# Optimization experiments

Measured on AMD Instinct MI355X. Metric: run time of the kernel, lower is better.

The kernel has to match this reference:

```python
import jax, jax.numpy as jnp
import numpy as np
import math

B, S, E, H, FF = 2, 2048, 1024, 16, 4096
HD = E // H
EPS = 1e-6


def layer_norm(x, gamma, beta):
    mu = jnp.mean(x, axis=-1, keepdims=True)
    var = jnp.mean(jnp.square(x - mu), axis=-1, keepdims=True)
    return (x - mu) * jax.lax.rsqrt(var + EPS) * gamma + beta


def setup_inputs() -> dict:
    key = jax.random.key(0)
    ks = jax.random.split(key, 8)
    x_embeds = jax.random.normal(ks[0], (B, S, E), dtype=jnp.float32)
    # causal mask: True means masked (j > i), broadcastable over batch/heads
    mask = jnp.triu(jnp.ones((S, S), dtype=bool), k=1)[None, None]
    sc = 1.0 / math.sqrt(E)
    w_kqv = jax.random.normal(ks[1], (3 * E, E), dtype=jnp.float32) * sc
    w_o = jax.random.normal(ks[2], (E, E), dtype=jnp.float32) * sc
    w_up = jax.random.normal(ks[3], (FF, E), dtype=jnp.float32) * sc
    b_up = jnp.zeros((FF,), dtype=jnp.float32)
    w_down = jax.random.normal(ks[4], (E, FF), dtype=jnp.float32) / math.sqrt(FF)
    b_down = jnp.zeros((E,), dtype=jnp.float32)
    g1 = jnp.ones((E,), dtype=jnp.float32)
    b1 = jnp.zeros((E,), dtype=jnp.float32)
    g2 = jnp.ones((E,), dtype=jnp.float32)
    b2 = jnp.zeros((E,), dtype=jnp.float32)
    return {"x_embeds": x_embeds, "mask": mask, "w_kqv": w_kqv, "w_o": w_o,
            "w_up": w_up, "b_up": b_up, "w_down": w_down, "b_down": b_down,
            "g1": g1, "b1": b1, "g2": g2, "b2": b2}


def reference(x_embeds, mask, w_kqv, w_o, w_up, b_up, w_down, b_down, g1, b1, g2, b2):
    b, s = x_embeds.shape[0], x_embeds.shape[1]
    # --- attention ---
    kqv = x_embeds @ w_kqv.T                      # [B,S,3E]
    kqv = kqv.reshape(b, s, 3, H, HD).transpose(0, 3, 2, 1, 4)  # [B,H,3,S,HD]
    xk, xq, xv = kqv[:, :, 0], kqv[:, :, 1], kqv[:, :, 2]
    attn = jnp.einsum('bhqd,bhkd->bhqk', xq, xk) / math.sqrt(HD)
    attn = jnp.where(mask, -jnp.inf, attn)
    attn = jax.nn.softmax(attn, axis=-1)
    out = jnp.einsum('bhqk,bhkd->bhqd', attn, xv)  # [B,H,S,HD]
    out = out.transpose(0, 2, 1, 3).reshape(b, s, E)
    out = out @ w_o.T
    x = layer_norm(out + x_embeds, g1, b1)
    # --- ffnn ---
    h = jax.nn.relu(x @ w_up.T + b_up)
    h = h @ w_down.T + b_down
    return layer_norm(h + x, g2, b2)
```

## Files before the change

### kernel.cpp

```cpp
#include <hip/hip_runtime.h>
#include <stdint.h>

#define B_ 2
#define S_ 2048
#define E_ 1024
#define H_ 16
#define HD_ 64
#define FF_ 4096
#define M_ 4096
#define LOG2E_ 1.44269504f

typedef short bf16x8 __attribute__((ext_vector_type(8)));
typedef float f32x4  __attribute__((ext_vector_type(4)));
typedef short shortx4 __attribute__((ext_vector_type(4)));

#define MFMA16(a,b,c) __builtin_amdgcn_mfma_f32_16x16x32_bf16(a,b,c,0,0,0)

__device__ __forceinline__ short f2bf(float f) {
  uint32_t u = __builtin_bit_cast(uint32_t, f);
  u += 0x7fffu + ((u >> 16) & 1u);
  return (short)(u >> 16);
}
__device__ __forceinline__ float bf2f(short b) {
  uint32_t u = ((uint32_t)(uint16_t)b) << 16;
  return __builtin_bit_cast(float, u);
}
__device__ __forceinline__ float exp2_hw(float x) {
  float r;
  asm("v_exp_f32 %0, %1" : "=v"(r) : "v"(x));
  return r;
}

template<int CTRL>
__device__ __forceinline__ float dpp_ror(float x) {
  return __builtin_bit_cast(float,
    __builtin_amdgcn_update_dpp(0, __builtin_bit_cast(int, x), CTRL, 0xF, 0xF, true));
}
__device__ __forceinline__ float dpp_max16(float v) {
  v = fmaxf(v, dpp_ror<0x128>(v));
  v = fmaxf(v, dpp_ror<0x124>(v));
  v = fmaxf(v, dpp_ror<0x122>(v));
  v = fmaxf(v, dpp_ror<0x121>(v));
  return v;
}
__device__ __forceinline__ float dpp_sum16(float v) {
  v += dpp_ror<0x128>(v);
  v += dpp_ror<0x124>(v);
  v += dpp_ror<0x122>(v);
  v += dpp_ror<0x121>(v);
  return v;
}

#define GLDS16(g, l) __builtin_amdgcn_global_load_lds( \
    (const __attribute__((address_space(1))) unsigned int*)(g), \
    (__attribute__((address_space(3))) unsigned int*)(l), 16, 0, 0)

__global__ void cast_all(const float* __restrict__ x, const float* __restrict__ wkqv,
                         const float* __restrict__ wo, const float* __restrict__ wup,
                         const float* __restrict__ wdown,
                         short* __restrict__ xb, short* __restrict__ wkqvb,
                         short* __restrict__ wob, short* __restrict__ wupb,
                         short* __restrict__ wdownb) {
  const int stride = gridDim.x * blockDim.x;
  for (int i = blockIdx.x * blockDim.x + threadIdx.x; i < 4194304; i += stride) {
    const int e = i << 2;
    const float* src; short* dst; int off;
    if (e < 4194304)       { src = x;     dst = xb;     off = e; }
    else if (e < 7340032)  { src = wkqv;  dst = wkqvb;  off = e - 4194304; }
    else if (e < 8388608)  { src = wo;    dst = wob;    off = e - 7340032; }
    else if (e < 12582912) { src = wup;   dst = wupb;   off = e - 8388608; }
    else                   { src = wdown; dst = wdownb; off = e - 12582912; }
    float4 v = *(const float4*)(src + off);
    shortx4 o;
    o.x = f2bf(v.x); o.y = f2bf(v.y); o.z = f2bf(v.z); o.w = f2bf(v.w);
    *(shortx4*)(dst + off) = o;
  }
}

template<int SK, int EPI, typename OutT>
__global__ __launch_bounds__(256) void gemm_bt(
    const short* __restrict__ A, const short* __restrict__ Bw,
    OutT* __restrict__ C0, OutT* __restrict__ C1, const float* __restrict__ bias,
    int M, int N, int K)
{
  __shared__ short Al[2][128 * 32];
  __shared__ short Bl[2][128 * 32];
  const int tid  = threadIdx.x;
  const int w    = tid >> 6, lane = tid & 63;
  const int ntiles = N >> 7;
  const int nwg = gridDim.x;
  const int bid = blockIdx.x;
  const int swz = (bid & 7) * (nwg >> 3) + (bid >> 3);
  const int tn = swz % ntiles, tm = swz / ntiles;
  const int m0 = tm << 7, n0 = tn << 7;
  const int wr = (w >> 1) << 6, wc = (w & 1) << 6;
  const int lr = lane & 15, lk = (lane >> 4) << 3;
  const int ra = lane >> 2, colA = (lane & 3) << 3;

  const int kper = K / SK;
  const int kbeg = (SK > 1) ? (int)blockIdx.y * kper : 0;
  const int T = kper >> 5;
  OutT* __restrict__ C = (SK > 1 && blockIdx.y) ? C1 : C0;

  const short* Ag0 = A  + (size_t)(m0 + w * 16 + ra) * K + colA;
  const short* Ag1 = A  + (size_t)(m0 + (w + 4) * 16 + ra) * K + colA;
  const short* Bg0 = Bw + (size_t)(n0 + w * 16 + ra) * K + colA;
  const short* Bg1 = Bw + (size_t)(n0 + (w + 4) * 16 + ra) * K + colA;

  f32x4 acc[4][4] = {};

  {
    const int k0 = kbeg;
    GLDS16(Ag0 + k0, &Al[0][w * 512]);
    GLDS16(Ag1 + k0, &Al[0][(w + 4) * 512]);
    GLDS16(Bg0 + k0, &Bl[0][w * 512]);
    GLDS16(Bg1 + k0, &Bl[0][(w + 4) * 512]);
  }

  for (int it = 0; it < T; ++it) {
    const int buf = it & 1;
    if (it + 1 < T) {
      const int k1 = kbeg + ((it + 1) << 5);
      GLDS16(Ag0 + k1, &Al[buf ^ 1][w * 512]);
      GLDS16(Ag1 + k1, &Al[buf ^ 1][(w + 4) * 512]);
      GLDS16(Bg0 + k1, &Bl[buf ^ 1][w * 512]);
      GLDS16(Bg1 + k1, &Bl[buf ^ 1][(w + 4) * 512]);
      asm volatile("s_waitcnt vmcnt(4)" ::: "memory");
    } else {
      asm volatile("s_waitcnt vmcnt(0)" ::: "memory");
    }
    __builtin_amdgcn_sched_barrier(0);
    __builtin_amdgcn_s_barrier();

    bf16x8 af[4], bfr[4];
    #pragma unroll
    for (int i = 0; i < 4; ++i)
      af[i] = *(const bf16x8*)&Al[buf][(wr + i * 16 + lr) * 32 + lk];
    #pragma unroll
    for (int j = 0; j < 4; ++j)
      bfr[j] = *(const bf16x8*)&Bl[buf][(wc + j * 16 + lr) * 32 + lk];
    #pragma unroll
    for (int i = 0; i < 4; ++i)
      #pragma unroll
      for (int j = 0; j < 4; ++j)
        acc[i][j] = MFMA16(af[i], bfr[j], acc[i][j]);

    __builtin_amdgcn_s_barrier();
  }

  const int lg = lane >> 4;
  #pragma unroll
  for (int j = 0; j < 4; ++j) {
    const int col = n0 + wc + j * 16 + lr;
    float bv = 0.f;
    if constexpr (SK == 1 && EPI != 0) bv = bias[col];
    #pragma unroll
    for (int i = 0; i < 4; ++i) {
      #pragma unroll
      for (int r = 0; r < 4; ++r) {
        const int row = m0 + wr + i * 16 + lg * 4 + r;
        float v = acc[i][j][r] + bv;
        if constexpr (SK == 1 && EPI == 1) v = fmaxf(v, 0.f);
        if constexpr (sizeof(OutT) == 2) C[(size_t)row * N + col] = f2bf(v);
        else                             C[(size_t)row * N + col] = v;
      }
    }
  }
}

__global__ __launch_bounds__(256) void attn_kernel(
    const short* __restrict__ kqv, short* __restrict__ out)
{
  __shared__ short Kt[64][72];
  __shared__ short Vt[64][72];
  __shared__ short Pl[4][16][72];

  const int tid = threadIdx.x, w = tid >> 6, lane = tid & 63;
  const int p = blockIdx.x;
  const int bh = blockIdx.y;
  const int b = bh >> 4, h = bh & 15;
  const int q0lo = p << 6, q0hi = (31 - p) << 6;
  const int nkb = 32 - p;
  const int lr = lane & 15, lg = lane >> 4;

  const size_t rowlo = (size_t)(b * S_ + q0lo + w * 16 + lr) * 3072 + 1024 + h * 64;
  const size_t rowhi = (size_t)(b * S_ + q0hi + w * 16 + lr) * 3072 + 1024 + h * 64;
  bf16x8 qlo[2], qhi[2];
  qlo[0] = *(const bf16x8*)&kqv[rowlo + lg * 8];
  qlo[1] = *(const bf16x8*)&kqv[rowlo + 32 + lg * 8];
  qhi[0] = *(const bf16x8*)&kqv[rowhi + lg * 8];
  qhi[1] = *(const bf16x8*)&kqv[rowhi + 32 + lg * 8];
  #pragma unroll
  for (int ks = 0; ks < 2; ++ks)
    #pragma unroll
    for (int e = 0; e < 8; ++e) {
      qlo[ks][e] = f2bf(bf2f(qlo[ks][e]) * 0.125f);
      qhi[ks][e] = f2bf(bf2f(qhi[ks][e]) * 0.125f);
    }

  f32x4 aclo[4] = {}, achi[4] = {};
  float mlo[4], llo[4], mhi[4], lhi[4];
  #pragma unroll
  for (int r = 0; r < 4; ++r) { mlo[r] = mhi[r] = -1e30f; llo[r] = lhi[r] = 0.f; }

  const int skk = tid >> 3;
  const int sc  = (tid & 7) << 3;
  const int vws = (tid & 7) << 3;

  for (int kbi = 0; kbi < nkb; ++kbi) {
    const int kb = kbi << 6;
    #pragma unroll
    for (int i = 0; i < 2; ++i) {
      const int krow = skk + i * 32;
      const size_t gb = (size_t)(b * S_ + kb + krow) * 3072 + h * 64 + sc;
      *(bf16x8*)&Kt[krow][sc] = *(const bf16x8*)&kqv[gb];
      bf16x8 vv = *(const bf16x8*)&kqv[gb + 2048];
      const int kc = krow ^ vws;
      #pragma unroll
      for (int e = 0; e < 8; ++e) Vt[sc + e][kc] = vv[e];
    }
    __syncthreads();

    auto process = [&](const bf16x8 (&qf)[2], f32x4 (&acc)[4],
                       float (&m_run)[4], float (&l_run)[4], int q0) {
      f32x4 sacc[4] = {};
      __builtin_amdgcn_s_setprio(1);
      #pragma unroll
      for (int jt = 0; jt < 4; ++jt) {
        #pragma unroll
        for (int ks = 0; ks < 2; ++ks) {
          bf16x8 kf = *(const bf16x8*)&Kt[jt * 16 + lr][ks * 32 + lg * 8];
          sacc[jt] = MFMA16(qf[ks], kf, sacc[jt]);
        }
      }
      __builtin_amdgcn_s_setprio(0);
      const bool full = (kb + 63 <= q0 + w * 16);
      float rmax[4];
      if (full) {
        #pragma unroll
        for (int r = 0; r < 4; ++r)
          rmax[r] = fmaxf(fmaxf(sacc[0][r], sacc[1][r]), fmaxf(sacc[2][r], sacc[3][r]));
      } else {
        #pragma unroll
        for (int r = 0; r < 4; ++r) rmax[r] = -1e30f;
        #pragma unroll
        for (int jt = 0; jt < 4; ++jt) {
          const int kpos = kb + jt * 16 + lr;
          #pragma unroll
          for (int r = 0; r < 4; ++r) {
            const int qrow = q0 + w * 16 + lg * 4 + r;
            float v = (kpos <= qrow) ? sacc[jt][r] : -1e30f;
            sacc[jt][r] = v;
            rmax[r] = fmaxf(rmax[r], v);
          }
        }
      }
      #pragma unroll
      for (int r = 0; r < 4; ++r) rmax[r] = dpp_max16(rmax[r]);
      int need = 0;
      #pragma unroll
      for (int r = 0; r < 4; ++r) need |= (rmax[r] > m_run[r] + 8.f) ? 1 : 0;
      if (__any(need)) {
        #pragma unroll
        for (int r = 0; r < 4; ++r) {
          const float mn = fmaxf(m_run[r], rmax[r]);
          const float al = exp2_hw((m_run[r] - mn) * LOG2E_);
          m_run[r] = mn;
          l_run[r] *= al;
          #pragma unroll
          for (int dt = 0; dt < 4; ++dt) acc[dt][r] *= al;
        }
      }
      float m2[4], rsum[4];
      #pragma unroll
      for (int r = 0; r < 4; ++r) { m2[r] = m_run[r] * LOG2E_; rsum[r] = 0.f; }
      #pragma unroll
      for (int jt = 0; jt < 4; ++jt)
        #pragma unroll
        for (int r = 0; r < 4; ++r) {
          const float pv = exp2_hw(__builtin_fmaf(sacc[jt][r], LOG2E_, -m2[r]));
          sacc[jt][r] = pv;
          rsum[r] += pv;
        }
      #pragma unroll
      for (int r = 0; r < 4; ++r) { rsum[r] = dpp_sum16(rsum[r]); l_run[r] += rsum[r]; }
      #pragma unroll
      for (int jt = 0; jt < 4; ++jt) {
        uint32_t w01, w23;
        asm("v_cvt_pk_bf16_f32 %0, %1, %2" : "=v"(w01) : "v"(sacc[jt][0]), "v"(sacc[jt][1]));
        asm("v_cvt_pk_bf16_f32 %0, %1, %2" : "=v"(w23) : "v"(sacc[jt][2]), "v"(sacc[jt][3]));
        Pl[w][lg * 4 + 0][jt * 16 + lr] = (short)(w01 & 0xffffu);
        Pl[w][lg * 4 + 1][jt * 16 + lr] = (short)(w01 >> 16);
        Pl[w][lg * 4 + 2][jt * 16 + lr] = (short)(w23 & 0xffffu);
        Pl[w][lg * 4 + 3][jt * 16 + lr] = (short)(w23 >> 16);
      }
      bf16x8 pa[2];
      pa[0] = *(const bf16x8*)&Pl[w][lr][lg * 8];
      pa[1] = *(const bf16x8*)&Pl[w][lr][32 + lg * 8];
      __builtin_amdgcn_s_setprio(1);
      #pragma unroll
      for (int dt = 0; dt < 4; ++dt) {
        const int vswz = (2 * dt + (lr >> 3)) << 3;
        #pragma unroll
        for (int ks = 0; ks < 2; ++ks) {
          bf16x8 vb = *(const bf16x8*)&Vt[dt * 16 + lr][(ks * 32 + lg * 8) ^ vswz];
          acc[dt] = MFMA16(pa[ks], vb, acc[dt]);
        }
      }
      __builtin_amdgcn_s_setprio(0);
    };

    process(qhi, achi, mhi, lhi, q0hi);
    if (kb <= q0lo + w * 16 + 15) process(qlo, aclo, mlo, llo, q0lo);
    __syncthreads();
  }

  #pragma unroll
  for (int dt = 0; dt < 4; ++dt) {
    #pragma unroll
    for (int r = 0; r < 4; ++r) {
      const int d = h * 64 + dt * 16 + lr;
      const int qlo_row = q0lo + w * 16 + lg * 4 + r;
      const int qhi_row = q0hi + w * 16 + lg * 4 + r;
      out[(size_t)(b * S_ + qlo_row) * E_ + d] = f2bf(aclo[dt][r] / llo[r]);
      out[(size_t)(b * S_ + qhi_row) * E_ + d] = f2bf(achi[dt][r] / lhi[r]);
    }
  }
}

template<int FINAL>
__global__ __launch_bounds__(256) void ln_kernel(
    const float* __restrict__ y0, const float* __restrict__ y1,
    const float* __restrict__ bias, const void* __restrict__ res,
    const float* __restrict__ gam, const float* __restrict__ bet,
    void* __restrict__ outp)
{
  const int row = blockIdx.x, tid = threadIdx.x, lane = tid & 63, w = tid >> 6;
  float4 a = ((const float4*)(y0 + (size_t)row * E_))[tid];
  float4 c = ((const float4*)(y1 + (size_t)row * E_))[tid];
  float r[4] = {a.x + c.x, a.y + c.y, a.z + c.z, a.w + c.w};
  if constexpr (FINAL) {
    float4 bi = ((const float4*)bias)[tid];
    shortx4 rb = ((const shortx4*)((const short*)res + (size_t)row * E_))[tid];
    r[0] += bi.x + bf2f(rb.x); r[1] += bi.y + bf2f(rb.y);
    r[2] += bi.z + bf2f(rb.z); r[3] += bi.w + bf2f(rb.w);
  } else {
    float4 rv = ((const float4*)((const float*)res + (size_t)row * E_))[tid];
    r[0] += rv.x; r[1] += rv.y; r[2] += rv.z; r[3] += rv.w;
  }
  float s  = r[0] + r[1] + r[2] + r[3];
  float ss = r[0]*r[0] + r[1]*r[1] + r[2]*r[2] + r[3]*r[3];
  #pragma unroll
  for (int m = 32; m >= 1; m >>= 1) { s += __shfl_xor(s, m); ss += __shfl_xor(ss, m); }
  __shared__ float red[8];
  if (lane == 0) { red[w] = s; red[4 + w] = ss; }
  __syncthreads();
  s  = red[0] + red[1] + red[2] + red[3];
  ss = red[4] + red[5] + red[6] + red[7];
  const float mu  = s * (1.f / E_);
  const float var = ss * (1.f / E_) - mu * mu;
  const float rs  = rsqrtf(var + 1e-6f);
  float4 gv = ((const float4*)gam)[tid];
  float4 bv = ((const float4*)bet)[tid];
  float o0 = (r[0] - mu) * rs * gv.x + bv.x;
  float o1 = (r[1] - mu) * rs * gv.y + bv.y;
  float o2 = (r[2] - mu) * rs * gv.z + bv.z;
  float o3 = (r[3] - mu) * rs * gv.w + bv.w;
  if constexpr (FINAL) {
    float4 o; o.x = o0; o.y = o1; o.z = o2; o.w = o3;
    ((float4*)((float*)outp + (size_t)row * E_))[tid] = o;
  } else {
    shortx4 o; o.x = f2bf(o0); o.y = f2bf(o1); o.z = f2bf(o2); o.w = f2bf(o3);
    ((shortx4*)((short*)outp + (size_t)row * E_))[tid] = o;
  }
}

extern "C" void kernel_launch(void* const* d_in, const int* in_sizes, int n_in,
                              void* d_out, int out_size, void* d_ws, size_t ws_size,
                              hipStream_t stream) {
  const float* x      = (const float*)d_in[0];
  const float* w_kqv  = (const float*)d_in[2];
  const float* w_o    = (const float*)d_in[3];
  const float* w_up   = (const float*)d_in[4];
  const float* b_up   = (const float*)d_in[5];
  const float* w_down = (const float*)d_in[6];
  const float* b_down = (const float*)d_in[7];
  const float* g1     = (const float*)d_in[8];
  const float* b1     = (const float*)d_in[9];
  const float* g2     = (const float*)d_in[10];
  const float* b2     = (const float*)d_in[11];
  float* out = (float*)d_out;

  char* ws = (char*)d_ws;
  short* xb     = (short*)(ws);
  short* wkqvb  = (short*)(ws + ((size_t)8  << 20));
  short* wob    = (short*)(ws + ((size_t)14 << 20));
  short* wupb   = (short*)(ws + ((size_t)16 << 20));
  short* wdownb = (short*)(ws + ((size_t)24 << 20));
  short* kqv    = (short*)(ws + ((size_t)32 << 20));
  float* proj0  = (float*)(ws + ((size_t)32 << 20));
  float* proj1  = (float*)(ws + ((size_t)48 << 20));
  short* hbuf   = (short*)(ws + ((size_t)32 << 20));
  short* attno  = (short*)(ws + ((size_t)64 << 20));
  short* xln    = (short*)(ws + ((size_t)72 << 20));
  float* down0  = (float*)(ws);
  float* down1  = (float*)(ws + ((size_t)80 << 20));

  cast_all<<<2048, 256, 0, stream>>>(x, w_kqv, w_o, w_up, w_down,
                                     xb, wkqvb, wob, wupb, wdownb);

  gemm_bt<1, 0, short><<<24 * 32, 256, 0, stream>>>(xb, wkqvb, kqv, nullptr, nullptr, M_, 3 * E_, E_);
  attn_kernel<<<dim3(16, B_ * H_), 256, 0, stream>>>(kqv, attno);
  gemm_bt<2, 0, float><<<dim3(256, 2), 256, 0, stream>>>(attno, wob, proj0, proj1, nullptr, M_, E_, E_);
  ln_kernel<0><<<M_, 256, 0, stream>>>(proj0, proj1, nullptr, x, g1, b1, xln);
  gemm_bt<1, 1, short><<<32 * 32, 256, 0, stream>>>(xln, wupb, hbuf, nullptr, b_up, M_, FF_, E_);
  gemm_bt<2, 0, float><<<dim3(256, 2), 256, 0, stream>>>(hbuf, wdownb, down0, down1, nullptr, M_, E_, FF_);
  ln_kernel<1><<<M_, 256, 0, stream>>>(down0, down1, b_down, xln, g2, b2, out);
}
```

Baseline: 257.4 us.

## Split paired causal attention blocks into one query tile per block, heaviest first

Before, each attention block handled a paired low and high query tile so that every block did equal causal work over shared K/V tiles. Now each block processes a single 64-row query tile, with twice as many blocks, and the block index is reversed so the longest tiles are scheduled first. This raises parallelism from 512 to 1024 blocks on the GPU and simplifies per-thread state. In exchange, each K/V tile load is no longer shared by two query tiles, and the work per block becomes unbalanced, which relies on the hardware scheduler to fill gaps.

```diff
diff --git a/kernel.cpp b/kernel.cpp
--- a/kernel.cpp
+++ b/kernel.cpp
@@ -176,32 +176,27 @@
   __shared__ short Pl[4][16][72];
 
   const int tid = threadIdx.x, w = tid >> 6, lane = tid & 63;
-  const int p = blockIdx.x;
+  const int p = 31 - blockIdx.x;
   const int bh = blockIdx.y;
   const int b = bh >> 4, h = bh & 15;
-  const int q0lo = p << 6, q0hi = (31 - p) << 6;
-  const int nkb = 32 - p;
+  const int q0 = p << 6;
+  const int nkb = p + 1;
   const int lr = lane & 15, lg = lane >> 4;
 
-  const size_t rowlo = (size_t)(b * S_ + q0lo + w * 16 + lr) * 3072 + 1024 + h * 64;
-  const size_t rowhi = (size_t)(b * S_ + q0hi + w * 16 + lr) * 3072 + 1024 + h * 64;
-  bf16x8 qlo[2], qhi[2];
-  qlo[0] = *(const bf16x8*)&kqv[rowlo + lg * 8];
-  qlo[1] = *(const bf16x8*)&kqv[rowlo + 32 + lg * 8];
-  qhi[0] = *(const bf16x8*)&kqv[rowhi + lg * 8];
-  qhi[1] = *(const bf16x8*)&kqv[rowhi + 32 + lg * 8];
+  const size_t rowq = (size_t)(b * S_ + q0 + w * 16 + lr) * 3072 + 1024 + h * 64;
+  bf16x8 qf[2];
+  qf[0] = *(const bf16x8*)&kqv[rowq + lg * 8];
+  qf[1] = *(const bf16x8*)&kqv[rowq + 32 + lg * 8];
   #pragma unroll
   for (int ks = 0; ks < 2; ++ks)
     #pragma unroll
-    for (int e = 0; e < 8; ++e) {
-      qlo[ks][e] = f2bf(bf2f(qlo[ks][e]) * 0.125f);
-      qhi[ks][e] = f2bf(bf2f(qhi[ks][e]) * 0.125f);
-    }
-
-  f32x4 aclo[4] = {}, achi[4] = {};
-  float mlo[4], llo[4], mhi[4], lhi[4];
+    for (int e = 0; e < 8; ++e)
+      qf[ks][e] = f2bf(bf2f(qf[ks][e]) * 0.125f);
+
+  f32x4 acc[4] = {};
+  float m_run[4], l_run[4];
   #pragma unroll
-  for (int r = 0; r < 4; ++r) { mlo[r] = mhi[r] = -1e30f; llo[r] = lhi[r] = 0.f; }
+  for (int r = 0; r < 4; ++r) { m_run[r] = -1e30f; l_run[r] = 0.f; }
 
   const int skk = tid >> 3;
   const int sc  = (tid & 7) << 3;
@@ -221,8 +216,7 @@
     }
     __syncthreads();
 
-    auto process = [&](const bf16x8 (&qf)[2], f32x4 (&acc)[4],
-                       float (&m_run)[4], float (&l_run)[4], int q0) {
+    {
       f32x4 sacc[4] = {};
       __builtin_amdgcn_s_setprio(1);
       #pragma unroll
@@ -308,10 +302,7 @@
         }
       }
       __builtin_amdgcn_s_setprio(0);
-    };
-
-    process(qhi, achi, mhi, lhi, q0hi);
-    if (kb <= q0lo + w * 16 + 15) process(qlo, aclo, mlo, llo, q0lo);
+    }
     __syncthreads();
   }
 
@@ -320,10 +311,8 @@
     #pragma unroll
     for (int r = 0; r < 4; ++r) {
       const int d = h * 64 + dt * 16 + lr;
-      const int qlo_row = q0lo + w * 16 + lg * 4 + r;
-      const int qhi_row = q0hi + w * 16 + lg * 4 + r;
-      out[(size_t)(b * S_ + qlo_row) * E_ + d] = f2bf(aclo[dt][r] / llo[r]);
-      out[(size_t)(b * S_ + qhi_row) * E_ + d] = f2bf(achi[dt][r] / lhi[r]);
+      const int q_row = q0 + w * 16 + lg * 4 + r;
+      out[(size_t)(b * S_ + q_row) * E_ + d] = f2bf(acc[dt][r] / l_run[r]);
     }
   }
 }
@@ -410,7 +399,7 @@
                                      xb, wkqvb, wob, wupb, wdownb);
 
   gemm_bt<1, 0, short><<<24 * 32, 256, 0, stream>>>(xb, wkqvb, kqv, nullptr, nullptr, M_, 3 * E_, E_);
-  attn_kernel<<<dim3(16, B_ * H_), 256, 0, stream>>>(kqv, attno);
+  attn_kernel<<<dim3(32, B_ * H_), 256, 0, stream>>>(kqv, attno);
   gemm_bt<2, 0, float><<<dim3(256, 2), 256, 0, stream>>>(attno, wob, proj0, proj1, nullptr, M_, E_, E_);
   ln_kernel<0><<<M_, 256, 0, stream>>>(proj0, proj1, nullptr, x, g1, b1, xln);
   gemm_bt<1, 1, short><<<32 * 32, 256, 0, stream>>>(xln, wupb, hbuf, nullptr, b_up, M_, FF_, E_);
```

Result: slower. 277.4 us (+7.8%).
